# Kernel tuning notes

Hardware: AMD Instinct MI355X
Metric: run time of the kernel (lower is better)

Reference implementation:

```python
import jax, jax.numpy as jnp
import numpy as np

UNITS = 1024

def setup_inputs() -> dict:
    key = jax.random.key(0)
    k1, k2, k3 = jax.random.split(key, 3)
    B, T, F = 32, 512, 1024
    scale_g = 1.0 / np.sqrt(F + UNITS)
    return {
        "inputs": jax.random.normal(k1, (B, T, F), dtype=jnp.float32),
        "gate_kernel": jax.random.normal(k2, (F + UNITS, 2 * UNITS), dtype=jnp.float32) * scale_g,
        "gate_bias": jnp.ones((2 * UNITS,), dtype=jnp.float32),  # TF GRUCell default gate bias = 1.0
        "cand_kernel": jax.random.normal(k3, (F + UNITS, UNITS), dtype=jnp.float32) * scale_g,
        "cand_bias": jnp.zeros((UNITS,), dtype=jnp.float32),
    }

def _gru_step(x, h, gate_kernel, gate_bias, cand_kernel, cand_bias):
    # TF GRUCell math: gates from [x, h], candidate from [x, r*h]
    xh = jnp.concatenate([x, h], axis=-1)                      # [B, F+U]
    gates = jax.nn.sigmoid(xh @ gate_kernel + gate_bias)       # [B, 2U]
    r, u = jnp.split(gates, 2, axis=-1)
    xrh = jnp.concatenate([x, r * h], axis=-1)
    c = jnp.tanh(xrh @ cand_kernel + cand_bias)                # [B, U]
    return u * h + (1.0 - u) * c

def reference(inputs, gate_kernel, gate_bias, cand_kernel, cand_bias):
    B = inputs.shape[0]
    h0 = jnp.zeros((B, UNITS), dtype=jnp.float32)  # cell.zero_state
    xs = jnp.swapaxes(inputs, 0, 1)                # [T, B, F] (unstack over time)

    def step(h, x):
        h_new = _gru_step(x, h, gate_kernel, gate_bias, cand_kernel, cand_bias)
        return h_new, h_new  # GRU output == new state

    _, ys = jax.lax.scan(step, h0, xs)             # ys: [T, B, U]
    return jnp.swapaxes(ys, 0, 1)                  # stack on axis=1 -> [B, T, U]
```

## Files before the change

kernel.cpp:

```cpp
#include <hip/hip_runtime.h>
#include <math.h>

#define BB 32
#define TT 512
#define FF 1024
#define UU 1024
#define NBLK 64

typedef __attribute__((ext_vector_type(8))) short s8v;
typedef __attribute__((ext_vector_type(4))) float f4v;
typedef __attribute__((ext_vector_type(2))) float f2v;
typedef __attribute__((ext_vector_type(2))) unsigned int u2v;

static __device__ __forceinline__ unsigned short f2bf(float f) {
    unsigned int u = __builtin_bit_cast(unsigned int, f);
    u += 0x7fff + ((u >> 16) & 1);
    return (unsigned short)(u >> 16);
}
static __device__ __forceinline__ float bf2f(unsigned short b) {
    unsigned int u = ((unsigned int)b) << 16;
    return __builtin_bit_cast(float, u);
}

static __device__ __forceinline__ s8v ld_b128_sc(const void* p) {
    s8v r;
    asm volatile("global_load_dwordx4 %0, %1, off sc0 sc1" : "=v"(r) : "v"(p));
    return r;
}
static __device__ __forceinline__ f4v ld_f128_sc(const void* p) {
    f4v r;
    asm volatile("global_load_dwordx4 %0, %1, off sc0 sc1" : "=v"(r) : "v"(p));
    return r;
}
static __device__ __forceinline__ f2v ld_f64_sc(const void* p) {
    f2v r;
    asm volatile("global_load_dwordx2 %0, %1, off sc0 sc1" : "=v"(r) : "v"(p));
    return r;
}
static __device__ __forceinline__ void st_b128_sc(void* p, f4v v) {
    asm volatile("global_store_dwordx4 %0, %1, off sc0 sc1" :: "v"(p), "v"(v));
}
static __device__ __forceinline__ void st_b64_sc(void* p, u2v v) {
    asm volatile("global_store_dwordx2 %0, %1, off sc0 sc1" :: "v"(p), "v"(v));
}
static __device__ __forceinline__ void st_f64_sc(void* p, f2v v) {
    asm volatile("global_store_dwordx2 %0, %1, off sc0 sc1" :: "v"(p), "v"(v));
}
static __device__ __forceinline__ void st_b32_sc(void* p, unsigned int v) {
    asm volatile("global_store_dword %0, %1, off sc0 sc1" :: "v"(p), "v"(v));
}
static __device__ __forceinline__ void vm_drain_schedfence() {
    asm volatile("s_waitcnt vmcnt(0)" ::: "memory");
    __builtin_amdgcn_sched_barrier(0);
}

__global__ __launch_bounds__(256) void cvt_bf16(
    const float* __restrict__ in, unsigned short* __restrict__ out, int n4)
{
    int i = blockIdx.x * 256 + threadIdx.x;
    if (i < n4) {
        float4 v = ((const float4*)in)[i];
        ushort4 o;
        o.x = f2bf(v.x); o.y = f2bf(v.y); o.z = f2bf(v.z); o.w = f2bf(v.w);
        ((ushort4*)out)[i] = o;
    }
}

template<int ROWS, int COLS>
__global__ __launch_bounds__(256) void transpose_bf16(
    const float* __restrict__ W, unsigned short* __restrict__ WT)
{
    __shared__ float tl[32][33];
    const int tx = threadIdx.x, ty = threadIdx.y;
    const int bx = blockIdx.x, by = blockIdx.y;
    #pragma unroll
    for (int i = 0; i < 4; ++i) {
        int r = by * 32 + ty + i * 8;
        int c = bx * 32 + tx;
        tl[ty + i * 8][tx] = W[(size_t)r * COLS + c];
    }
    __syncthreads();
    #pragma unroll
    for (int i = 0; i < 4; ++i) {
        int n = bx * 32 + ty + i * 8;
        int k = by * 32 + tx;
        WT[(size_t)n * ROWS + k] = f2bf(tl[tx][ty + i * 8]);
    }
}

__global__ __launch_bounds__(256) void gemm_xproj(
    const unsigned short* __restrict__ A,
    const unsigned short* __restrict__ BT,
    unsigned short* __restrict__ C,
    int N)
{
    __shared__ unsigned short Al[128][72];
    __shared__ unsigned short Bl[128][72];
    const int tid  = threadIdx.x;
    const int lane = tid & 63;
    const int wave = tid >> 6;
    const int l15  = lane & 15;
    const int kg   = lane >> 4;
    const int m0   = blockIdx.y * 128;
    const int n0   = blockIdx.x * 128;
    const int rowOff = (wave >> 1) * 64;
    const int colOff = (wave & 1) * 64;

    f4v acc[4][4];
    #pragma unroll
    for (int m = 0; m < 4; ++m)
        #pragma unroll
        for (int n = 0; n < 4; ++n) acc[m][n] = (f4v){0.f, 0.f, 0.f, 0.f};

    for (int k0 = 0; k0 < 1024; k0 += 64) {
        #pragma unroll
        for (int it = 0; it < 4; ++it) {
            int c = tid + it * 256;
            int r = c >> 3, off = (c & 7) * 8;
            *(s8v*)&Al[r][off] = *(const s8v*)(A + (size_t)(m0 + r) * 1024 + k0 + off);
            *(s8v*)&Bl[r][off] = *(const s8v*)(BT + (size_t)(n0 + r) * 2048 + k0 + off);
        }
        __syncthreads();
        #pragma unroll
        for (int ks = 0; ks < 2; ++ks) {
            s8v a[4], b[4];
            #pragma unroll
            for (int m = 0; m < 4; ++m)
                a[m] = *(const s8v*)&Al[rowOff + m * 16 + l15][ks * 32 + kg * 8];
            #pragma unroll
            for (int n = 0; n < 4; ++n)
                b[n] = *(const s8v*)&Bl[colOff + n * 16 + l15][ks * 32 + kg * 8];
            #pragma unroll
            for (int m = 0; m < 4; ++m)
                #pragma unroll
                for (int n = 0; n < 4; ++n)
                    acc[m][n] = __builtin_amdgcn_mfma_f32_16x16x32_bf16(a[m], b[n], acc[m][n], 0, 0, 0);
        }
        __syncthreads();
    }
    #pragma unroll
    for (int m = 0; m < 4; ++m)
        #pragma unroll
        for (int n = 0; n < 4; ++n)
            #pragma unroll
            for (int i = 0; i < 4; ++i) {
                int row = m0 + rowOff + m * 16 + kg * 4 + i;
                int col = n0 + colOff + n * 16 + l15;
                C[(size_t)row * N + col] = f2bf(acc[m][n][i]);
            }
}

__device__ __forceinline__ void grid_barrier(unsigned* counter, unsigned target, int tid)
{
    asm volatile("s_waitcnt vmcnt(0)" ::: "memory");
    __syncthreads();
    if (tid == 0) {
        __hip_atomic_fetch_add(counter, 1u, __ATOMIC_RELAXED, __HIP_MEMORY_SCOPE_AGENT);
        while (__hip_atomic_load(counter, __ATOMIC_RELAXED, __HIP_MEMORY_SCOPE_AGENT) < target)
            __builtin_amdgcn_s_sleep(1);
    }
    __syncthreads();
}

__global__ __launch_bounds__(256, 1) void gru_persistent(
    const unsigned short* __restrict__ WgT,
    const unsigned short* __restrict__ WcT,
    const unsigned short* __restrict__ Xgb,
    const unsigned short* __restrict__ Xcb,
    const float* __restrict__ bg,
    const float* __restrict__ bc,
    float* __restrict__ h,
    unsigned short* __restrict__ hb,
    unsigned short* __restrict__ rhb,
    float* __restrict__ ub,
    float* __restrict__ out,
    unsigned* __restrict__ bar)
{
    __shared__ float red[4][32][32];
    __shared__ unsigned short wc_l[16 * 1024];
    const int tid  = threadIdx.x;
    const int lane = tid & 63;
    const int wave = tid >> 6;
    const int l15  = lane & 15;
    const int kg   = lane >> 4;
    const int blk  = blockIdx.x;
    const int gj0  = blk * 32;
    const int cj0  = blk * 16;
    const int kb   = wave * 256;
    const bool is_r = (gj0 < UU);

    #pragma unroll
    for (int it = 0; it < 8; ++it) {
        int c   = tid + it * 256;
        int col = c >> 7;
        int k   = (c & 127) * 8;
        s8v w = *(const s8v*)(WcT + (size_t)(cj0 + col) * 2048 + 1024 + k);
        *(s8v*)&wc_l[col * 1024 + (k ^ ((col & 7) << 3))] = w;
    }

    s8v bgf[2][8];
    #pragma unroll
    for (int n = 0; n < 2; ++n)
        #pragma unroll
        for (int kk = 0; kk < 8; ++kk)
            bgf[n][kk] = *(const s8v*)(WgT + (size_t)(gj0 + n * 16 + l15) * 2048
                                            + 1024 + kb + kk * 32 + kg * 8);

    const int eb = tid >> 3;
    const int eq = tid & 7;
    const float4 bgv = *(const float4*)(bg + gj0 + eq * 4);
    const float2 bcv = *(const float2*)(bc + cj0 + eq * 2);

    __syncthreads();

    unsigned epoch = 0;
    ushort4 xg = *(const ushort4*)(Xgb + ((size_t)eb * TT + 0) * 2048 + gj0 + eq * 4);

    for (int t = 0; t < TT; ++t) {
        f4v hsl = (f4v){0.f,0.f,0.f,0.f};
        if (is_r) hsl = ld_f128_sc(h + eb * UU + gj0 + eq * 4);

        s8v a[2][8];
        #pragma unroll
        for (int m = 0; m < 2; ++m)
            #pragma unroll
            for (int kk = 0; kk < 8; ++kk)
                a[m][kk] = ld_b128_sc(hb + (size_t)(m * 16 + l15) * 1024 + kb + kk * 32 + kg * 8);
        vm_drain_schedfence();

        f4v acc[2][2];
        #pragma unroll
        for (int m = 0; m < 2; ++m)
            #pragma unroll
            for (int n = 0; n < 2; ++n) acc[m][n] = (f4v){0.f, 0.f, 0.f, 0.f};
        #pragma unroll
        for (int kk = 0; kk < 8; ++kk)
            #pragma unroll
            for (int m = 0; m < 2; ++m)
                #pragma unroll
                for (int n = 0; n < 2; ++n)
                    acc[m][n] = __builtin_amdgcn_mfma_f32_16x16x32_bf16(a[m][kk], bgf[n][kk], acc[m][n], 0, 0, 0);

        #pragma unroll
        for (int m = 0; m < 2; ++m)
            #pragma unroll
            for (int n = 0; n < 2; ++n)
                #pragma unroll
                for (int i = 0; i < 4; ++i)
                    red[wave][m * 16 + kg * 4 + i][n * 16 + l15] = acc[m][n][i];
        __syncthreads();

        f4v pre = *(const f4v*)&red[0][eb][eq * 4];
        #pragma unroll
        for (int w = 1; w < 4; ++w) pre += *(const f4v*)&red[w][eb][eq * 4];
        pre[0] += bf2f(xg.x) + bgv.x;
        pre[1] += bf2f(xg.y) + bgv.y;
        pre[2] += bf2f(xg.z) + bgv.z;
        pre[3] += bf2f(xg.w) + bgv.w;
        float s0 = 1.f / (1.f + __expf(-pre[0]));
        float s1 = 1.f / (1.f + __expf(-pre[1]));
        float s2 = 1.f / (1.f + __expf(-pre[2]));
        float s3 = 1.f / (1.f + __expf(-pre[3]));
        if (is_r) {
            unsigned int lo = (unsigned int)f2bf(s0 * hsl[0]) | ((unsigned int)f2bf(s1 * hsl[1]) << 16);
            unsigned int hi = (unsigned int)f2bf(s2 * hsl[2]) | ((unsigned int)f2bf(s3 * hsl[3]) << 16);
            st_b64_sc(rhb + eb * UU + gj0 + eq * 4, (u2v){lo, hi});
        } else {
            st_b128_sc(ub + eb * UU + (gj0 - UU) + eq * 4, (f4v){s0, s1, s2, s3});
        }

        ushort2 xc = *(const ushort2*)(Xcb + ((size_t)eb * TT + t) * 1024 + cj0 + eq * 2);
        f2v hv = ld_f64_sc(h + eb * UU + cj0 + eq * 2);

        ++epoch;
        grid_barrier(bar, epoch * NBLK, tid);

        f2v uv = ld_f64_sc(ub + eb * UU + cj0 + eq * 2);

        s8v ac[2][8];
        #pragma unroll
        for (int m = 0; m < 2; ++m)
            #pragma unroll
            for (int kk = 0; kk < 8; ++kk)
                ac[m][kk] = ld_b128_sc(rhb + (size_t)(m * 16 + l15) * 1024 + kb + kk * 32 + kg * 8);
        vm_drain_schedfence();

        f4v acc2[2];
        acc2[0] = (f4v){0.f, 0.f, 0.f, 0.f};
        acc2[1] = (f4v){0.f, 0.f, 0.f, 0.f};
        #pragma unroll
        for (int kk = 0; kk < 8; ++kk) {
            s8v bcf = *(const s8v*)&wc_l[l15 * 1024 + ((kb + kk * 32 + kg * 8) ^ ((l15 & 7) << 3))];
            #pragma unroll
            for (int m = 0; m < 2; ++m)
                acc2[m] = __builtin_amdgcn_mfma_f32_16x16x32_bf16(ac[m][kk], bcf, acc2[m], 0, 0, 0);
        }

        float* redc = (float*)red;
        #pragma unroll
        for (int m = 0; m < 2; ++m)
            #pragma unroll
            for (int i = 0; i < 4; ++i)
                redc[((size_t)wave * 32 + m * 16 + kg * 4 + i) * 16 + l15] = acc2[m][i];
        __syncthreads();

        float2 pre2 = *(const float2*)&redc[(0 * 32 + eb) * 16 + eq * 2];
        #pragma unroll
        for (int w = 1; w < 4; ++w) {
            float2 p = *(const float2*)&redc[((size_t)w * 32 + eb) * 16 + eq * 2];
            pre2.x += p.x; pre2.y += p.y;
        }
        float c0 = pre2.x + bf2f(xc.x) + bcv.x;
        float c1 = pre2.y + bf2f(xc.y) + bcv.y;
        c0 = fminf(fmaxf(c0, -15.f), 15.f);
        c1 = fminf(fmaxf(c1, -15.f), 15.f);
        float e0 = __expf(2.f * c0), e1 = __expf(2.f * c1);
        float t0 = (e0 - 1.f) / (e0 + 1.f);
        float t1 = (e1 - 1.f) / (e1 + 1.f);
        float hn0 = uv[0] * hv[0] + (1.f - uv[0]) * t0;
        float hn1 = uv[1] * hv[1] + (1.f - uv[1]) * t1;

        st_f64_sc(h + eb * UU + cj0 + eq * 2, (f2v){hn0, hn1});
        st_b32_sc(hb + eb * UU + cj0 + eq * 2,
                  (unsigned int)f2bf(hn0) | ((unsigned int)f2bf(hn1) << 16));
        *(float2*)(out + ((size_t)eb * TT + t) * UU + cj0 + eq * 2) = make_float2(hn0, hn1);

        if (t + 1 < TT)
            xg = *(const ushort4*)(Xgb + ((size_t)eb * TT + t + 1) * 2048 + gj0 + eq * 4);

        ++epoch;
        if (t + 1 < TT) grid_barrier(bar, epoch * NBLK, tid);
    }
}

__global__ __launch_bounds__(256) void gru_gates2(
    const unsigned short* __restrict__ hb, const unsigned short* __restrict__ WgT,
    const unsigned short* __restrict__ Xgb, const float* __restrict__ bg,
    const float* __restrict__ h, unsigned short* __restrict__ rhb,
    float* __restrict__ ubuf, int t)
{
    __shared__ unsigned short hb_l[32][1032];
    __shared__ unsigned short Wl[16][1032];
    __shared__ float red[4][32][16];
    const int tid = threadIdx.x, lane = tid & 63, wave = tid >> 6;
    const int l15 = lane & 15, kg = lane >> 4;
    const int j0 = blockIdx.x * 16;
    #pragma unroll
    for (int it = 0; it < 16; ++it) {
        int c = tid + it * 256; int r = c >> 7, off = (c & 127) * 8;
        *(s8v*)&hb_l[r][off] = *(const s8v*)(hb + (size_t)r * 1024 + off);
    }
    #pragma unroll
    for (int it = 0; it < 8; ++it) {
        int c = tid + it * 256; int r = c >> 7, off = (c & 127) * 8;
        *(s8v*)&Wl[r][off] = *(const s8v*)(WgT + (size_t)(j0 + r) * 2048 + 1024 + off);
    }
    __syncthreads();
    f4v acc0 = (f4v){0.f,0.f,0.f,0.f}, acc1 = (f4v){0.f,0.f,0.f,0.f};
    const int kbase = wave * 256;
    #pragma unroll
    for (int kk = 0; kk < 8; ++kk) {
        int k = kbase + kk * 32 + kg * 8;
        s8v a0 = *(const s8v*)&hb_l[l15][k];
        s8v a1 = *(const s8v*)&hb_l[16 + l15][k];
        s8v b  = *(const s8v*)&Wl[l15][k];
        acc0 = __builtin_amdgcn_mfma_f32_16x16x32_bf16(a0, b, acc0, 0, 0, 0);
        acc1 = __builtin_amdgcn_mfma_f32_16x16x32_bf16(a1, b, acc1, 0, 0, 0);
    }
    #pragma unroll
    for (int i = 0; i < 4; ++i) {
        red[wave][kg * 4 + i][l15] = acc0[i];
        red[wave][16 + kg * 4 + i][l15] = acc1[i];
    }
    __syncthreads();
    for (int e = tid; e < 512; e += 256) {
        int b = e >> 4, col = e & 15;
        int j = j0 + col;
        float pre = red[0][b][col] + red[1][b][col] + red[2][b][col] + red[3][b][col];
        pre += bf2f(Xgb[((size_t)b * TT + t) * 2048 + j]) + bg[j];
        float s = 1.f / (1.f + __expf(-pre));
        if (j < UU) rhb[b * UU + j] = f2bf(s * h[b * UU + j]);
        else        ubuf[b * UU + (j - UU)] = s;
    }
}

__global__ __launch_bounds__(256) void gru_cand2(
    const unsigned short* __restrict__ rhb, const unsigned short* __restrict__ WcT,
    const unsigned short* __restrict__ Xcb, const float* __restrict__ bc,
    const float* __restrict__ ubuf, float* __restrict__ h,
    unsigned short* __restrict__ hb, float* __restrict__ out, int t)
{
    __shared__ unsigned short rh_l[32][1032];
    __shared__ unsigned short Wl[16][1032];
    __shared__ float red[4][32][16];
    const int tid = threadIdx.x, lane = tid & 63, wave = tid >> 6;
    const int l15 = lane & 15, kg = lane >> 4;
    const int j0 = blockIdx.x * 16;
    #pragma unroll
    for (int it = 0; it < 16; ++it) {
        int c = tid + it * 256; int r = c >> 7, off = (c & 127) * 8;
        *(s8v*)&rh_l[r][off] = *(const s8v*)(rhb + (size_t)r * 1024 + off);
    }
    #pragma unroll
    for (int it = 0; it < 8; ++it) {
        int c = tid + it * 256; int r = c >> 7, off = (c & 127) * 8;
        *(s8v*)&Wl[r][off] = *(const s8v*)(WcT + (size_t)(j0 + r) * 2048 + 1024 + off);
    }
    __syncthreads();
    f4v acc0 = (f4v){0.f,0.f,0.f,0.f}, acc1 = (f4v){0.f,0.f,0.f,0.f};
    const int kbase = wave * 256;
    #pragma unroll
    for (int kk = 0; kk < 8; ++kk) {
        int k = kbase + kk * 32 + kg * 8;
        s8v a0 = *(const s8v*)&rh_l[l15][k];
        s8v a1 = *(const s8v*)&rh_l[16 + l15][k];
        s8v b  = *(const s8v*)&Wl[l15][k];
        acc0 = __builtin_amdgcn_mfma_f32_16x16x32_bf16(a0, b, acc0, 0, 0, 0);
        acc1 = __builtin_amdgcn_mfma_f32_16x16x32_bf16(a1, b, acc1, 0, 0, 0);
    }
    #pragma unroll
    for (int i = 0; i < 4; ++i) {
        red[wave][kg * 4 + i][l15] = acc0[i];
        red[wave][16 + kg * 4 + i][l15] = acc1[i];
    }
    __syncthreads();
    for (int e = tid; e < 512; e += 256) {
        int b = e >> 4, col = e & 15;
        int j = j0 + col;
        float pre = red[0][b][col] + red[1][b][col] + red[2][b][col] + red[3][b][col];
        pre += bf2f(Xcb[((size_t)b * TT + t) * 1024 + j]) + bc[j];
        float cv = tanhf(pre);
        float u  = ubuf[b * UU + j];
        float hv = h[b * UU + j];
        float hn = u * hv + (1.f - u) * cv;
        h[b * UU + j]  = hn;
        hb[b * UU + j] = f2bf(hn);
        out[((size_t)b * TT + t) * UU + j] = hn;
    }
}

extern "C" void kernel_launch(void* const* d_in, const int* in_sizes, int n_in,
                              void* d_out, int out_size, void* d_ws, size_t ws_size,
                              hipStream_t stream) {
    const float* x  = (const float*)d_in[0];
    const float* Wg = (const float*)d_in[1];
    const float* bg = (const float*)d_in[2];
    const float* Wc = (const float*)d_in[3];
    const float* bc = (const float*)d_in[4];
    float* out = (float*)d_out;

    const size_t XB_B  = (size_t)BB * TT * FF * 2;
    const size_t WGT_B = (size_t)2 * UU * (FF + UU) * 2;
    const size_t WCT_B = (size_t)UU * (FF + UU) * 2;
    const size_t XG_B  = (size_t)BB * TT * 2 * UU * 2;
    const size_t XC_B  = (size_t)BB * TT * UU * 2;
    const size_t H_B   = (size_t)BB * UU * 4;
    const size_t HB_B  = (size_t)BB * UU * 2;
    const size_t BAR_B = 256;
    const size_t NEED  = XB_B + WGT_B + WCT_B + XG_B + XC_B + H_B + HB_B * 2 + H_B + BAR_B;

    char* p = (char*)d_ws;
    unsigned short* xb  = (unsigned short*)p;            p += XB_B;
    unsigned short* WgT = (unsigned short*)p;            p += WGT_B;
    unsigned short* WcT = (unsigned short*)p;            p += WCT_B;
    unsigned short* Xgb = (unsigned short*)p;            p += XG_B;
    unsigned short* Xcb = (unsigned short*)p;            p += XC_B;
    float*          h   = (float*)p;                     p += H_B;
    unsigned short* hb  = (unsigned short*)p;            p += HB_B;
    unsigned short* rhb = (unsigned short*)p;            p += HB_B;
    float*          ub  = (float*)p;                     p += H_B;
    unsigned*       bar = (unsigned*)p;                  p += BAR_B;

    cvt_bf16<<<(BB * TT * FF / 4 + 255) / 256, 256, 0, stream>>>(x, xb, BB * TT * FF / 4);
    transpose_bf16<FF + UU, 2 * UU><<<dim3(64, 64), dim3(32, 8), 0, stream>>>(Wg, WgT);
    transpose_bf16<FF + UU, UU>    <<<dim3(32, 64), dim3(32, 8), 0, stream>>>(Wc, WcT);
    gemm_xproj<<<dim3(2 * UU / 128, BB * TT / 128), 256, 0, stream>>>(xb, WgT, Xgb, 2 * UU);
    gemm_xproj<<<dim3(UU / 128,     BB * TT / 128), 256, 0, stream>>>(xb, WcT, Xcb, UU);
    hipMemsetAsync(h,   0, H_B,   stream);
    hipMemsetAsync(hb,  0, HB_B,  stream);
    hipMemsetAsync(bar, 0, BAR_B, stream);

    if (ws_size >= NEED) {
        gru_persistent<<<NBLK, 256, 0, stream>>>(WgT, WcT, Xgb, Xcb, bg, bc,
                                                 h, hb, rhb, ub, out, bar);
    } else {
        for (int t = 0; t < TT; ++t) {
            gru_gates2<<<128, 256, 0, stream>>>(hb, WgT, Xgb, bg, h, rhb, ub, t);
            gru_cand2 <<< 64, 256, 0, stream>>>(rhb, WcT, Xcb, bc, ub, h, hb, out, t);
        }
    }
}
```

Measured before the change: 4.774 ms.

## Split persistent GRU into batch groups with per-group barriers

```diff
diff --git a/kernel.cpp b/kernel.cpp
--- a/kernel.cpp
+++ b/kernel.cpp
@@ -5,7 +5,10 @@
 #define TT 512
 #define FF 1024
 #define UU 1024
-#define NBLK 64
+#define NGRP 4
+#define GBLK 16
+#define MROW 8
+#define NBLK (NGRP * GBLK)
 
 typedef __attribute__((ext_vector_type(8))) short s8v;
 typedef __attribute__((ext_vector_type(4))) float f4v;
@@ -150,7 +153,7 @@
             }
 }
 
-__device__ __forceinline__ void grid_barrier(unsigned* counter, unsigned target, int tid)
+__device__ __forceinline__ void group_barrier(unsigned* counter, unsigned target, int tid)
 {
     asm volatile("s_waitcnt vmcnt(0)" ::: "memory");
     __syncthreads();
@@ -176,160 +179,155 @@
     float* __restrict__ out,
     unsigned* __restrict__ bar)
 {
-    __shared__ float red[4][32][32];
-    __shared__ unsigned short wc_l[16 * 1024];
+    __shared__ float red[4][8][8][16];
     const int tid  = threadIdx.x;
     const int lane = tid & 63;
     const int wave = tid >> 6;
     const int l15  = lane & 15;
     const int kg   = lane >> 4;
-    const int blk  = blockIdx.x;
-    const int gj0  = blk * 32;
-    const int cj0  = blk * 16;
+    const int grp  = blockIdx.x >> 4;
+    const int gb   = blockIdx.x & 15;
+    const int b0   = grp * MROW;
+    const int gj0  = gb * 128;
+    const int cj0  = gb * 64;
     const int kb   = wave * 256;
-    const bool is_r = (gj0 < UU);
-
-    #pragma unroll
-    for (int it = 0; it < 8; ++it) {
-        int c   = tid + it * 256;
-        int col = c >> 7;
-        int k   = (c & 127) * 8;
-        s8v w = *(const s8v*)(WcT + (size_t)(cj0 + col) * 2048 + 1024 + k);
-        *(s8v*)&wc_l[col * 1024 + (k ^ ((col & 7) << 3))] = w;
-    }
-
-    s8v bgf[2][8];
-    #pragma unroll
-    for (int n = 0; n < 2; ++n)
+    const bool is_r = (gb < 8);
+    unsigned* cnt  = bar + grp * 64;
+
+    const int arow = b0 + (l15 & 7);
+
+    const int erow = tid >> 5;
+    const int ecg  = tid & 31;
+    const int eb   = b0 + erow;
+    const int gc   = ecg * 4;
+    const int cc2  = ecg * 2;
+
+    const float4 bgv = *(const float4*)(bg + gj0 + gc);
+    const float2 bcv = *(const float2*)(bc + cj0 + cc2);
+
+    unsigned epoch = 0;
+
+    for (int t = 0; t < TT; ++t) {
+        f4v hsl = (f4v){0.f, 0.f, 0.f, 0.f};
+        if (is_r) hsl = ld_f128_sc(h + (size_t)eb * UU + gj0 + gc);
+
+        s8v a[8];
         #pragma unroll
         for (int kk = 0; kk < 8; ++kk)
-            bgf[n][kk] = *(const s8v*)(WgT + (size_t)(gj0 + n * 16 + l15) * 2048
+            a[kk] = ld_b128_sc(hb + (size_t)arow * UU + kb + kk * 32 + kg * 8);
+        vm_drain_schedfence();
+
+        f4v acc[8];
+        #pragma unroll
+        for (int n = 0; n < 8; ++n) acc[n] = (f4v){0.f, 0.f, 0.f, 0.f};
+        #pragma unroll
+        for (int n = 0; n < 8; ++n) {
+            s8v bf[8];
+            #pragma unroll
+            for (int kk = 0; kk < 8; ++kk)
+                bf[kk] = *(const s8v*)(WgT + (size_t)(gj0 + n * 16 + l15) * 2048
                                             + 1024 + kb + kk * 32 + kg * 8);
-
-    const int eb = tid >> 3;
-    const int eq = tid & 7;
-    const float4 bgv = *(const float4*)(bg + gj0 + eq * 4);
-    const float2 bcv = *(const float2*)(bc + cj0 + eq * 2);
-
-    __syncthreads();
-
-    unsigned epoch = 0;
-    ushort4 xg = *(const ushort4*)(Xgb + ((size_t)eb * TT + 0) * 2048 + gj0 + eq * 4);
-
-    for (int t = 0; t < TT; ++t) {
-        f4v hsl = (f4v){0.f,0.f,0.f,0.f};
-        if (is_r) hsl = ld_f128_sc(h + eb * UU + gj0 + eq * 4);
-
-        s8v a[2][8];
-        #pragma unroll
-        for (int m = 0; m < 2; ++m)
             #pragma unroll
             for (int kk = 0; kk < 8; ++kk)
-                a[m][kk] = ld_b128_sc(hb + (size_t)(m * 16 + l15) * 1024 + kb + kk * 32 + kg * 8);
-        vm_drain_schedfence();
-
-        f4v acc[2][2];
-        #pragma unroll
-        for (int m = 0; m < 2; ++m)
-            #pragma unroll
-            for (int n = 0; n < 2; ++n) acc[m][n] = (f4v){0.f, 0.f, 0.f, 0.f};
-        #pragma unroll
-        for (int kk = 0; kk < 8; ++kk)
-            #pragma unroll
-            for (int m = 0; m < 2; ++m)
-                #pragma unroll
-                for (int n = 0; n < 2; ++n)
-                    acc[m][n] = __builtin_amdgcn_mfma_f32_16x16x32_bf16(a[m][kk], bgf[n][kk], acc[m][n], 0, 0, 0);
-
-        #pragma unroll
-        for (int m = 0; m < 2; ++m)
-            #pragma unroll
-            for (int n = 0; n < 2; ++n)
+                acc[n] = __builtin_amdgcn_mfma_f32_16x16x32_bf16(a[kk], bf[kk], acc[n], 0, 0, 0);
+        }
+
+        if (kg < 2) {
+            #pragma unroll
+            for (int n = 0; n < 8; ++n)
                 #pragma unroll
                 for (int i = 0; i < 4; ++i)
-                    red[wave][m * 16 + kg * 4 + i][n * 16 + l15] = acc[m][n][i];
+                    red[wave][n][kg * 4 + i][l15] = acc[n][i];
+        }
         __syncthreads();
 
-        f4v pre = *(const f4v*)&red[0][eb][eq * 4];
-        #pragma unroll
-        for (int w = 1; w < 4; ++w) pre += *(const f4v*)&red[w][eb][eq * 4];
-        pre[0] += bf2f(xg.x) + bgv.x;
-        pre[1] += bf2f(xg.y) + bgv.y;
-        pre[2] += bf2f(xg.z) + bgv.z;
-        pre[3] += bf2f(xg.w) + bgv.w;
-        float s0 = 1.f / (1.f + __expf(-pre[0]));
-        float s1 = 1.f / (1.f + __expf(-pre[1]));
-        float s2 = 1.f / (1.f + __expf(-pre[2]));
-        float s3 = 1.f / (1.f + __expf(-pre[3]));
-        if (is_r) {
-            unsigned int lo = (unsigned int)f2bf(s0 * hsl[0]) | ((unsigned int)f2bf(s1 * hsl[1]) << 16);
-            unsigned int hi = (unsigned int)f2bf(s2 * hsl[2]) | ((unsigned int)f2bf(s3 * hsl[3]) << 16);
-            st_b64_sc(rhb + eb * UU + gj0 + eq * 4, (u2v){lo, hi});
-        } else {
-            st_b128_sc(ub + eb * UU + (gj0 - UU) + eq * 4, (f4v){s0, s1, s2, s3});
-        }
-
-        ushort2 xc = *(const ushort2*)(Xcb + ((size_t)eb * TT + t) * 1024 + cj0 + eq * 2);
-        f2v hv = ld_f64_sc(h + eb * UU + cj0 + eq * 2);
+        {
+            const int n = gc >> 4, cw = gc & 15;
+            f4v pre = *(const f4v*)&red[0][n][erow][cw];
+            #pragma unroll
+            for (int w = 1; w < 4; ++w) pre += *(const f4v*)&red[w][n][erow][cw];
+            ushort4 xg = *(const ushort4*)(Xgb + ((size_t)eb * TT + t) * 2048 + gj0 + gc);
+            pre[0] += bf2f(xg.x) + bgv.x;
+            pre[1] += bf2f(xg.y) + bgv.y;
+            pre[2] += bf2f(xg.z) + bgv.z;
+            pre[3] += bf2f(xg.w) + bgv.w;
+            float s0 = 1.f / (1.f + __expf(-pre[0]));
+            float s1 = 1.f / (1.f + __expf(-pre[1]));
+            float s2 = 1.f / (1.f + __expf(-pre[2]));
+            float s3 = 1.f / (1.f + __expf(-pre[3]));
+            if (is_r) {
+                unsigned int lo = (unsigned int)f2bf(s0 * hsl[0]) | ((unsigned int)f2bf(s1 * hsl[1]) << 16);
+                unsigned int hi = (unsigned int)f2bf(s2 * hsl[2]) | ((unsigned int)f2bf(s3 * hsl[3]) << 16);
+                st_b64_sc(rhb + (size_t)eb * UU + gj0 + gc, (u2v){lo, hi});
+            } else {
+                st_b128_sc(ub + (size_t)eb * UU + (gj0 - UU) + gc, (f4v){s0, s1, s2, s3});
+            }
+        }
+
+        ushort2 xc = *(const ushort2*)(Xcb + ((size_t)eb * TT + t) * 1024 + cj0 + cc2);
+        f2v hv = ld_f64_sc(h + (size_t)eb * UU + cj0 + cc2);
 
         ++epoch;
-        grid_barrier(bar, epoch * NBLK, tid);
-
-        f2v uv = ld_f64_sc(ub + eb * UU + cj0 + eq * 2);
-
-        s8v ac[2][8];
-        #pragma unroll
-        for (int m = 0; m < 2; ++m)
+        group_barrier(cnt, epoch * GBLK, tid);
+
+        f2v uv = ld_f64_sc(ub + (size_t)eb * UU + cj0 + cc2);
+
+        s8v ac[8];
+        #pragma unroll
+        for (int kk = 0; kk < 8; ++kk)
+            ac[kk] = ld_b128_sc(rhb + (size_t)arow * UU + kb + kk * 32 + kg * 8);
+        vm_drain_schedfence();
+
+        f4v acc2[4];
+        #pragma unroll
+        for (int n = 0; n < 4; ++n) acc2[n] = (f4v){0.f, 0.f, 0.f, 0.f};
+        #pragma unroll
+        for (int n = 0; n < 4; ++n) {
+            s8v bf[8];
             #pragma unroll
             for (int kk = 0; kk < 8; ++kk)
-                ac[m][kk] = ld_b128_sc(rhb + (size_t)(m * 16 + l15) * 1024 + kb + kk * 32 + kg * 8);
-        vm_drain_schedfence();
-
-        f4v acc2[2];
-        acc2[0] = (f4v){0.f, 0.f, 0.f, 0.f};
-        acc2[1] = (f4v){0.f, 0.f, 0.f, 0.f};
-        #pragma unroll
-        for (int kk = 0; kk < 8; ++kk) {
-            s8v bcf = *(const s8v*)&wc_l[l15 * 1024 + ((kb + kk * 32 + kg * 8) ^ ((l15 & 7) << 3))];
-            #pragma unroll
-            for (int m = 0; m < 2; ++m)
-                acc2[m] = __builtin_amdgcn_mfma_f32_16x16x32_bf16(ac[m][kk], bcf, acc2[m], 0, 0, 0);
-        }
-
-        float* redc = (float*)red;
-        #pragma unroll
-        for (int m = 0; m < 2; ++m)
-            #pragma unroll
-            for (int i = 0; i < 4; ++i)
-                redc[((size_t)wave * 32 + m * 16 + kg * 4 + i) * 16 + l15] = acc2[m][i];
+                bf[kk] = *(const s8v*)(WcT + (size_t)(cj0 + n * 16 + l15) * 2048
+                                            + 1024 + kb + kk * 32 + kg * 8);
+            #pragma unroll
+            for (int kk = 0; kk < 8; ++kk)
+                acc2[n] = __builtin_amdgcn_mfma_f32_16x16x32_bf16(ac[kk], bf[kk], acc2[n], 0, 0, 0);
+        }
+
+        if (kg < 2) {
+            #pragma unroll
+            for (int n = 0; n < 4; ++n)
+                #pragma unroll
+                for (int i = 0; i < 4; ++i)
+                    red[wave][n][kg * 4 + i][l15] = acc2[n][i];
+        }
         __syncthreads();
 
-        float2 pre2 = *(const float2*)&redc[(0 * 32 + eb) * 16 + eq * 2];
-        #pragma unroll
-        for (int w = 1; w < 4; ++w) {
-            float2 p = *(const float2*)&redc[((size_t)w * 32 + eb) * 16 + eq * 2];
-            pre2.x += p.x; pre2.y += p.y;
-        }
-        float c0 = pre2.x + bf2f(xc.x) + bcv.x;
-        float c1 = pre2.y + bf2f(xc.y) + bcv.y;
-        c0 = fminf(fmaxf(c0, -15.f), 15.f);
-        c1 = fminf(fmaxf(c1, -15.f), 15.f);
-        float e0 = __expf(2.f * c0), e1 = __expf(2.f * c1);
-        float t0 = (e0 - 1.f) / (e0 + 1.f);
-        float t1 = (e1 - 1.f) / (e1 + 1.f);
-        float hn0 = uv[0] * hv[0] + (1.f - uv[0]) * t0;
-        float hn1 = uv[1] * hv[1] + (1.f - uv[1]) * t1;
-
-        st_f64_sc(h + eb * UU + cj0 + eq * 2, (f2v){hn0, hn1});
-        st_b32_sc(hb + eb * UU + cj0 + eq * 2,
-                  (unsigned int)f2bf(hn0) | ((unsigned int)f2bf(hn1) << 16));
-        *(float2*)(out + ((size_t)eb * TT + t) * UU + cj0 + eq * 2) = make_float2(hn0, hn1);
-
-        if (t + 1 < TT)
-            xg = *(const ushort4*)(Xgb + ((size_t)eb * TT + t + 1) * 2048 + gj0 + eq * 4);
+        {
+            const int n = cc2 >> 4, cw = cc2 & 15;
+            f2v pre2 = *(const f2v*)&red[0][n][erow][cw];
+            #pragma unroll
+            for (int w = 1; w < 4; ++w) {
+                f2v p = *(const f2v*)&red[w][n][erow][cw];
+                pre2[0] += p[0]; pre2[1] += p[1];
+            }
+            float c0 = pre2[0] + bf2f(xc.x) + bcv.x;
+            float c1 = pre2[1] + bf2f(xc.y) + bcv.y;
+            c0 = fminf(fmaxf(c0, -15.f), 15.f);
+            c1 = fminf(fmaxf(c1, -15.f), 15.f);
+            float e0 = __expf(2.f * c0), e1 = __expf(2.f * c1);
+            float t0 = (e0 - 1.f) / (e0 + 1.f);
+            float t1 = (e1 - 1.f) / (e1 + 1.f);
+            float hn0 = uv[0] * hv[0] + (1.f - uv[0]) * t0;
+            float hn1 = uv[1] * hv[1] + (1.f - uv[1]) * t1;
+
+            st_f64_sc(h + (size_t)eb * UU + cj0 + cc2, (f2v){hn0, hn1});
+            st_b32_sc(hb + (size_t)eb * UU + cj0 + cc2,
+                      (unsigned int)f2bf(hn0) | ((unsigned int)f2bf(hn1) << 16));
+            *(float2*)(out + ((size_t)eb * TT + t) * UU + cj0 + cc2) = make_float2(hn0, hn1);
+        }
 
         ++epoch;
-        if (t + 1 < TT) grid_barrier(bar, epoch * NBLK, tid);
+        if (t + 1 < TT) group_barrier(cnt, epoch * GBLK, tid);
     }
 }
 
@@ -456,7 +454,7 @@
     const size_t XC_B  = (size_t)BB * TT * UU * 2;
     const size_t H_B   = (size_t)BB * UU * 4;
     const size_t HB_B  = (size_t)BB * UU * 2;
-    const size_t BAR_B = 256;
+    const size_t BAR_B = 4096;
     const size_t NEED  = XB_B + WGT_B + WCT_B + XG_B + XC_B + H_B + HB_B * 2 + H_B + BAR_B;
 
     char* p = (char*)d_ws;
```

Result: slower. 8.880 ms (+86.0%).

## Split batch into two halves with independent barrier counters to overlap GRU phases

Applied to the files above, without the earlier changes.

```diff
diff --git a/kernel.cpp b/kernel.cpp
--- a/kernel.cpp
+++ b/kernel.cpp
@@ -6,11 +6,11 @@
 #define FF 1024
 #define UU 1024
 #define NBLK 64
+#define MR 16
 
 typedef __attribute__((ext_vector_type(8))) short s8v;
 typedef __attribute__((ext_vector_type(4))) float f4v;
 typedef __attribute__((ext_vector_type(2))) float f2v;
-typedef __attribute__((ext_vector_type(2))) unsigned int u2v;
 
 static __device__ __forceinline__ unsigned short f2bf(float f) {
     unsigned int u = __builtin_bit_cast(unsigned int, f);
@@ -27,27 +27,27 @@
     asm volatile("global_load_dwordx4 %0, %1, off sc0 sc1" : "=v"(r) : "v"(p));
     return r;
 }
-static __device__ __forceinline__ f4v ld_f128_sc(const void* p) {
-    f4v r;
-    asm volatile("global_load_dwordx4 %0, %1, off sc0 sc1" : "=v"(r) : "v"(p));
-    return r;
-}
 static __device__ __forceinline__ f2v ld_f64_sc(const void* p) {
     f2v r;
     asm volatile("global_load_dwordx2 %0, %1, off sc0 sc1" : "=v"(r) : "v"(p));
     return r;
 }
-static __device__ __forceinline__ void st_b128_sc(void* p, f4v v) {
-    asm volatile("global_store_dwordx4 %0, %1, off sc0 sc1" :: "v"(p), "v"(v));
-}
-static __device__ __forceinline__ void st_b64_sc(void* p, u2v v) {
-    asm volatile("global_store_dwordx2 %0, %1, off sc0 sc1" :: "v"(p), "v"(v));
+static __device__ __forceinline__ float ld_f32_sc(const void* p) {
+    float r;
+    asm volatile("global_load_dword %0, %1, off sc0 sc1" : "=v"(r) : "v"(p));
+    return r;
 }
 static __device__ __forceinline__ void st_f64_sc(void* p, f2v v) {
     asm volatile("global_store_dwordx2 %0, %1, off sc0 sc1" :: "v"(p), "v"(v));
 }
 static __device__ __forceinline__ void st_b32_sc(void* p, unsigned int v) {
     asm volatile("global_store_dword %0, %1, off sc0 sc1" :: "v"(p), "v"(v));
+}
+static __device__ __forceinline__ void st_f32_sc(void* p, float v) {
+    asm volatile("global_store_dword %0, %1, off sc0 sc1" :: "v"(p), "v"(v));
+}
+static __device__ __forceinline__ void st_u16_sc(void* p, unsigned int v) {
+    asm volatile("global_store_short %0, %1, off sc0 sc1" :: "v"(p), "v"(v));
 }
 static __device__ __forceinline__ void vm_drain_schedfence() {
     asm volatile("s_waitcnt vmcnt(0)" ::: "memory");
@@ -150,18 +150,6 @@
             }
 }
 
-__device__ __forceinline__ void grid_barrier(unsigned* counter, unsigned target, int tid)
-{
-    asm volatile("s_waitcnt vmcnt(0)" ::: "memory");
-    __syncthreads();
-    if (tid == 0) {
-        __hip_atomic_fetch_add(counter, 1u, __ATOMIC_RELAXED, __HIP_MEMORY_SCOPE_AGENT);
-        while (__hip_atomic_load(counter, __ATOMIC_RELAXED, __HIP_MEMORY_SCOPE_AGENT) < target)
-            __builtin_amdgcn_s_sleep(1);
-    }
-    __syncthreads();
-}
-
 __global__ __launch_bounds__(256, 1) void gru_persistent(
     const unsigned short* __restrict__ WgT,
     const unsigned short* __restrict__ WcT,
@@ -176,7 +164,7 @@
     float* __restrict__ out,
     unsigned* __restrict__ bar)
 {
-    __shared__ float red[4][32][32];
+    __shared__ float red[4][2][16][16];
     __shared__ unsigned short wc_l[16 * 1024];
     const int tid  = threadIdx.x;
     const int lane = tid & 63;
@@ -188,6 +176,8 @@
     const int cj0  = blk * 16;
     const int kb   = wave * 256;
     const bool is_r = (gj0 < UU);
+    unsigned* cA = bar;
+    unsigned* cB = bar + 64;
 
     #pragma unroll
     for (int it = 0; it < 8; ++it) {
@@ -206,130 +196,127 @@
             bgf[n][kk] = *(const s8v*)(WgT + (size_t)(gj0 + n * 16 + l15) * 2048
                                             + 1024 + kb + kk * 32 + kg * 8);
 
-    const int eb = tid >> 3;
-    const int eq = tid & 7;
-    const float4 bgv = *(const float4*)(bg + gj0 + eq * 4);
-    const float2 bcv = *(const float2*)(bc + cj0 + eq * 2);
-
-    __syncthreads();
-
-    unsigned epoch = 0;
-    ushort4 xg = *(const ushort4*)(Xgb + ((size_t)eb * TT + 0) * 2048 + gj0 + eq * 4);
-
-    for (int t = 0; t < TT; ++t) {
-        f4v hsl = (f4v){0.f,0.f,0.f,0.f};
-        if (is_r) hsl = ld_f128_sc(h + eb * UU + gj0 + eq * 4);
-
-        s8v a[2][8];
-        #pragma unroll
-        for (int m = 0; m < 2; ++m)
+    const int erow = tid >> 4;
+    const int ecp  = tid & 15;
+    const float2 bgv = *(const float2*)(bg + gj0 + ecp * 2);
+    const float  bcs = bc[cj0 + ecp];
+
+    __syncthreads();
+
+    auto arrive = [&](unsigned* cnt) {
+        asm volatile("s_waitcnt vmcnt(0)" ::: "memory");
+        __syncthreads();
+        if (tid == 0)
+            __hip_atomic_fetch_add(cnt, 1u, __ATOMIC_RELAXED, __HIP_MEMORY_SCOPE_AGENT);
+    };
+    auto wait = [&](unsigned* cnt, unsigned tgt) {
+        if (tid == 0)
+            while (__hip_atomic_load(cnt, __ATOMIC_RELAXED, __HIP_MEMORY_SCOPE_AGENT) < tgt)
+                __builtin_amdgcn_s_sleep(1);
+        __syncthreads();
+    };
+
+    int t = 0;
+    float hvA = 0.f, hvB = 0.f;
+    unsigned short xcA = 0, xcB = 0;
+    ushort2 xgA = *(const ushort2*)(Xgb + ((size_t)(0  + erow) * TT) * 2048 + gj0 + ecp * 2);
+    ushort2 xgB = *(const ushort2*)(Xgb + ((size_t)(MR + erow) * TT) * 2048 + gj0 + ecp * 2);
+
+    auto phaseG = [&](int b0, ushort2 xg, float& hv, unsigned short& xc, unsigned* cnt) {
+        xc = Xcb[((size_t)(b0 + erow) * TT + t) * 1024 + cj0 + ecp];
+        hv = ld_f32_sc(h + (size_t)(b0 + erow) * UU + cj0 + ecp);
+        f2v hsl = (f2v){0.f, 0.f};
+        if (is_r) hsl = ld_f64_sc(h + (size_t)(b0 + erow) * UU + gj0 + ecp * 2);
+
+        s8v a[8];
+        #pragma unroll
+        for (int kk = 0; kk < 8; ++kk)
+            a[kk] = ld_b128_sc(hb + (size_t)(b0 + l15) * UU + kb + kk * 32 + kg * 8);
+        vm_drain_schedfence();
+
+        f4v acc[2];
+        acc[0] = (f4v){0.f, 0.f, 0.f, 0.f};
+        acc[1] = (f4v){0.f, 0.f, 0.f, 0.f};
+        #pragma unroll
+        for (int kk = 0; kk < 8; ++kk) {
+            acc[0] = __builtin_amdgcn_mfma_f32_16x16x32_bf16(a[kk], bgf[0][kk], acc[0], 0, 0, 0);
+            acc[1] = __builtin_amdgcn_mfma_f32_16x16x32_bf16(a[kk], bgf[1][kk], acc[1], 0, 0, 0);
+        }
+        #pragma unroll
+        for (int n = 0; n < 2; ++n)
             #pragma unroll
-            for (int kk = 0; kk < 8; ++kk)
-                a[m][kk] = ld_b128_sc(hb + (size_t)(m * 16 + l15) * 1024 + kb + kk * 32 + kg * 8);
+            for (int i = 0; i < 4; ++i)
+                red[wave][n][kg * 4 + i][l15] = acc[n][i];
+        __syncthreads();
+
+        const int n = ecp >> 3, cw = (ecp & 7) * 2;
+        float2 pre = *(const float2*)&red[0][n][erow][cw];
+        #pragma unroll
+        for (int w = 1; w < 4; ++w) {
+            float2 p = *(const float2*)&red[w][n][erow][cw];
+            pre.x += p.x; pre.y += p.y;
+        }
+        pre.x += bf2f(xg.x) + bgv.x;
+        pre.y += bf2f(xg.y) + bgv.y;
+        float s0 = 1.f / (1.f + __expf(-pre.x));
+        float s1 = 1.f / (1.f + __expf(-pre.y));
+        if (is_r) {
+            unsigned int packed = (unsigned int)f2bf(s0 * hsl[0])
+                                | ((unsigned int)f2bf(s1 * hsl[1]) << 16);
+            st_b32_sc(rhb + (size_t)(b0 + erow) * UU + gj0 + ecp * 2, packed);
+        } else {
+            st_f64_sc(ub + (size_t)(b0 + erow) * UU + (gj0 - UU) + ecp * 2, (f2v){s0, s1});
+        }
+        arrive(cnt);
+    };
+
+    auto phaseC = [&](int b0, float hv, unsigned short xc, ushort2& xg, unsigned* cnt) {
+        float uv = ld_f32_sc(ub + (size_t)(b0 + erow) * UU + cj0 + ecp);
+        s8v ac[8];
+        #pragma unroll
+        for (int kk = 0; kk < 8; ++kk)
+            ac[kk] = ld_b128_sc(rhb + (size_t)(b0 + l15) * UU + kb + kk * 32 + kg * 8);
+        int tn = (t + 1 < TT) ? t + 1 : t;
+        xg = *(const ushort2*)(Xgb + ((size_t)(b0 + erow) * TT + tn) * 2048 + gj0 + ecp * 2);
         vm_drain_schedfence();
 
-        f4v acc[2][2];
-        #pragma unroll
-        for (int m = 0; m < 2; ++m)
-            #pragma unroll
-            for (int n = 0; n < 2; ++n) acc[m][n] = (f4v){0.f, 0.f, 0.f, 0.f};
-        #pragma unroll
-        for (int kk = 0; kk < 8; ++kk)
-            #pragma unroll
-            for (int m = 0; m < 2; ++m)
-                #pragma unroll
-                for (int n = 0; n < 2; ++n)
-                    acc[m][n] = __builtin_amdgcn_mfma_f32_16x16x32_bf16(a[m][kk], bgf[n][kk], acc[m][n], 0, 0, 0);
-
-        #pragma unroll
-        for (int m = 0; m < 2; ++m)
-            #pragma unroll
-            for (int n = 0; n < 2; ++n)
-                #pragma unroll
-                for (int i = 0; i < 4; ++i)
-                    red[wave][m * 16 + kg * 4 + i][n * 16 + l15] = acc[m][n][i];
-        __syncthreads();
-
-        f4v pre = *(const f4v*)&red[0][eb][eq * 4];
-        #pragma unroll
-        for (int w = 1; w < 4; ++w) pre += *(const f4v*)&red[w][eb][eq * 4];
-        pre[0] += bf2f(xg.x) + bgv.x;
-        pre[1] += bf2f(xg.y) + bgv.y;
-        pre[2] += bf2f(xg.z) + bgv.z;
-        pre[3] += bf2f(xg.w) + bgv.w;
-        float s0 = 1.f / (1.f + __expf(-pre[0]));
-        float s1 = 1.f / (1.f + __expf(-pre[1]));
-        float s2 = 1.f / (1.f + __expf(-pre[2]));
-        float s3 = 1.f / (1.f + __expf(-pre[3]));
-        if (is_r) {
-            unsigned int lo = (unsigned int)f2bf(s0 * hsl[0]) | ((unsigned int)f2bf(s1 * hsl[1]) << 16);
-            unsigned int hi = (unsigned int)f2bf(s2 * hsl[2]) | ((unsigned int)f2bf(s3 * hsl[3]) << 16);
-            st_b64_sc(rhb + eb * UU + gj0 + eq * 4, (u2v){lo, hi});
-        } else {
-            st_b128_sc(ub + eb * UU + (gj0 - UU) + eq * 4, (f4v){s0, s1, s2, s3});
-        }
-
-        ushort2 xc = *(const ushort2*)(Xcb + ((size_t)eb * TT + t) * 1024 + cj0 + eq * 2);
-        f2v hv = ld_f64_sc(h + eb * UU + cj0 + eq * 2);
-
-        ++epoch;
-        grid_barrier(bar, epoch * NBLK, tid);
-
-        f2v uv = ld_f64_sc(ub + eb * UU + cj0 + eq * 2);
-
-        s8v ac[2][8];
-        #pragma unroll
-        for (int m = 0; m < 2; ++m)
-            #pragma unroll
-            for (int kk = 0; kk < 8; ++kk)
-                ac[m][kk] = ld_b128_sc(rhb + (size_t)(m * 16 + l15) * 1024 + kb + kk * 32 + kg * 8);
-        vm_drain_schedfence();
-
-        f4v acc2[2];
-        acc2[0] = (f4v){0.f, 0.f, 0.f, 0.f};
-        acc2[1] = (f4v){0.f, 0.f, 0.f, 0.f};
+        f4v acc2 = (f4v){0.f, 0.f, 0.f, 0.f};
         #pragma unroll
         for (int kk = 0; kk < 8; ++kk) {
             s8v bcf = *(const s8v*)&wc_l[l15 * 1024 + ((kb + kk * 32 + kg * 8) ^ ((l15 & 7) << 3))];
-            #pragma unroll
-            for (int m = 0; m < 2; ++m)
-                acc2[m] = __builtin_amdgcn_mfma_f32_16x16x32_bf16(ac[m][kk], bcf, acc2[m], 0, 0, 0);
-        }
-
+            acc2 = __builtin_amdgcn_mfma_f32_16x16x32_bf16(ac[kk], bcf, acc2, 0, 0, 0);
+        }
         float* redc = (float*)red;
         #pragma unroll
-        for (int m = 0; m < 2; ++m)
-            #pragma unroll
-            for (int i = 0; i < 4; ++i)
-                redc[((size_t)wave * 32 + m * 16 + kg * 4 + i) * 16 + l15] = acc2[m][i];
-        __syncthreads();
-
-        float2 pre2 = *(const float2*)&redc[(0 * 32 + eb) * 16 + eq * 2];
-        #pragma unroll
-        for (int w = 1; w < 4; ++w) {
-            float2 p = *(const float2*)&redc[((size_t)w * 32 + eb) * 16 + eq * 2];
-            pre2.x += p.x; pre2.y += p.y;
-        }
-        float c0 = pre2.x + bf2f(xc.x) + bcv.x;
-        float c1 = pre2.y + bf2f(xc.y) + bcv.y;
-        c0 = fminf(fmaxf(c0, -15.f), 15.f);
-        c1 = fminf(fmaxf(c1, -15.f), 15.f);
-        float e0 = __expf(2.f * c0), e1 = __expf(2.f * c1);
-        float t0 = (e0 - 1.f) / (e0 + 1.f);
-        float t1 = (e1 - 1.f) / (e1 + 1.f);
-        float hn0 = uv[0] * hv[0] + (1.f - uv[0]) * t0;
-        float hn1 = uv[1] * hv[1] + (1.f - uv[1]) * t1;
-
-        st_f64_sc(h + eb * UU + cj0 + eq * 2, (f2v){hn0, hn1});
-        st_b32_sc(hb + eb * UU + cj0 + eq * 2,
-                  (unsigned int)f2bf(hn0) | ((unsigned int)f2bf(hn1) << 16));
-        *(float2*)(out + ((size_t)eb * TT + t) * UU + cj0 + eq * 2) = make_float2(hn0, hn1);
-
-        if (t + 1 < TT)
-            xg = *(const ushort4*)(Xgb + ((size_t)eb * TT + t + 1) * 2048 + gj0 + eq * 4);
-
-        ++epoch;
-        if (t + 1 < TT) grid_barrier(bar, epoch * NBLK, tid);
+        for (int i = 0; i < 4; ++i)
+            redc[((size_t)wave * 16 + kg * 4 + i) * 16 + l15] = acc2[i];
+        __syncthreads();
+
+        float pre = redc[(0 * 16 + erow) * 16 + ecp];
+        #pragma unroll
+        for (int w = 1; w < 4; ++w) pre += redc[((size_t)w * 16 + erow) * 16 + ecp];
+        float cv = pre + bf2f(xc) + bcs;
+        cv = fminf(fmaxf(cv, -15.f), 15.f);
+        float e = __expf(2.f * cv);
+        float th = (e - 1.f) / (e + 1.f);
+        float hn = uv * hv + (1.f - uv) * th;
+
+        st_f32_sc(h + (size_t)(b0 + erow) * UU + cj0 + ecp, hn);
+        st_u16_sc(hb + (size_t)(b0 + erow) * UU + cj0 + ecp, (unsigned int)f2bf(hn));
+        out[((size_t)(b0 + erow) * TT + t) * UU + cj0 + ecp] = hn;
+        arrive(cnt);
+    };
+
+    for (t = 0; t < TT; ++t) {
+        const unsigned base = (unsigned)(2 * t) * NBLK;
+        wait(cA, base);
+        phaseG(0, xgA, hvA, xcA, cA);
+        wait(cB, base);
+        phaseG(MR, xgB, hvB, xcB, cB);
+        wait(cA, base + NBLK);
+        phaseC(0, hvA, xcA, xgA, cA);
+        wait(cB, base + NBLK);
+        phaseC(MR, hvB, xcB, xgB, cB);
     }
 }
 
@@ -456,7 +443,7 @@
     const size_t XC_B  = (size_t)BB * TT * UU * 2;
     const size_t H_B   = (size_t)BB * UU * 4;
     const size_t HB_B  = (size_t)BB * UU * 2;
-    const size_t BAR_B = 256;
+    const size_t BAR_B = 4096;
     const size_t NEED  = XB_B + WGT_B + WCT_B + XG_B + XC_B + H_B + HB_B * 2 + H_B + BAR_B;
 
     char* p = (char*)d_ws;
```

New measurement: 5.204 ms. 9.0% more time.
